# Performance work log

Measured on AMD Instinct MI355X. Metric: run time of the kernel, lower is better.

## Reference

```python
import jax, jax.numpy as jnp
import numpy as np

B, H, W = 8, 64, 64
DIM1, DIM2 = 384, 256
NH, DH = 8, 32
INNER = NH * DH
EPS = 1e-5


def _layernorm(x, w, b):
    mu = jnp.mean(x, axis=-1, keepdims=True)
    var = jnp.mean((x - mu) ** 2, axis=-1, keepdims=True)
    return (x - mu) * jax.lax.rsqrt(var + EPS) * w + b


def _axial_attn(q, k, v, scale):
    # q,k,v: [B,H,W,nh,dh]; row attention over H, col attention over W
    sh = jnp.einsum('biwnd,bjwnd->bwnij', q, k) * scale  # [B,W,nh,H,H]
    oh = jnp.einsum('bwnij,bjwnd->biwnd', jax.nn.softmax(sh, axis=-1), v)
    sw = jnp.einsum('bhind,bhjnd->bhnij', q, k) * scale  # [B,H,nh,W,W]
    ow = jnp.einsum('bhnij,bhjnd->bhind', jax.nn.softmax(sw, axis=-1), v)
    return oh + ow  # [B,H,W,nh,dh]


def setup_inputs() -> dict:
    key = jax.random.key(0)
    ks = jax.random.split(key, 16)
    s1 = 1.0 / np.sqrt(DIM1)
    s2 = 1.0 / np.sqrt(DIM2)
    si = 1.0 / np.sqrt(INNER)
    return {
        'x1': jax.random.normal(ks[0], (B, DIM1, H, W), jnp.float32),
        'x2': jax.random.normal(ks[1], (B, DIM2, H, W), jnp.float32),
        'ln1q_w': jnp.ones((DIM1,), jnp.float32),
        'ln1q_b': jnp.zeros((DIM1,), jnp.float32),
        'ln2kv_w': jnp.ones((DIM2,), jnp.float32),
        'ln2kv_b': jnp.zeros((DIM2,), jnp.float32),
        'Wq1': jax.random.normal(ks[2], (DIM1, INNER), jnp.float32) * s1,
        'Wkv2': jax.random.normal(ks[3], (DIM2, 2 * INNER), jnp.float32) * s2,
        'Wout1': jax.random.normal(ks[4], (INNER, DIM2), jnp.float32) * si,
        'bout1': jnp.zeros((DIM2,), jnp.float32),
        'ln2q_w': jnp.ones((DIM2,), jnp.float32),
        'ln2q_b': jnp.zeros((DIM2,), jnp.float32),
        'ln1kv_w': jnp.ones((DIM1,), jnp.float32),
        'ln1kv_b': jnp.zeros((DIM1,), jnp.float32),
        'Wq2': jax.random.normal(ks[5], (DIM2, INNER), jnp.float32) * s2,
        'Wkv1': jax.random.normal(ks[6], (DIM1, 2 * INNER), jnp.float32) * s1,
        'Wout2': jax.random.normal(ks[7], (INNER, DIM2), jnp.float32) * si,
        'bout2': jnp.zeros((DIM2,), jnp.float32),
        'Wsc': jax.random.normal(ks[8], (DIM2, DIM1), jnp.float32) * s1,  # 1x1 conv [out,in]
        'bn_gamma': jnp.ones((DIM2,), jnp.float32),
        'bn_beta': jnp.zeros((DIM2,), jnp.float32),
        'bn_mean': jnp.zeros((DIM2,), jnp.float32),
        'bn_var': jnp.ones((DIM2,), jnp.float32),
    }


def reference(x1, x2, ln1q_w, ln1q_b, ln2kv_w, ln2kv_b, Wq1, Wkv2, Wout1, bout1,
              ln2q_w, ln2q_b, ln1kv_w, ln1kv_b, Wq2, Wkv1, Wout2, bout2,
              Wsc, bn_gamma, bn_beta, bn_mean, bn_var):
    b, c1, h, w = x1.shape
    scale = DH ** -0.5
    x1f = jnp.transpose(x1, (0, 2, 3, 1))  # [B,H,W,C1]
    x2f = jnp.transpose(x2, (0, 2, 3, 1))  # [B,H,W,C2]

    def heads(t):
        return t.reshape(b, h, w, NH, DH)

    # branch 1: q from x1, kv from x2
    q1 = _layernorm(x1f, ln1q_w, ln1q_b) @ Wq1
    kv2 = _layernorm(x2f, ln2kv_w, ln2kv_b) @ Wkv2
    k2, v2 = jnp.split(kv2, 2, axis=-1)
    o1 = _axial_attn(heads(q1), heads(k2), heads(v2), scale)
    fused1 = o1.reshape(b, h, w, INNER) @ Wout1 + bout1
    # shortcut: 1x1 conv + BN (inference stats)
    sc = jnp.einsum('bhwc,oc->bhwo', x1f, Wsc)
    sc = (sc - bn_mean) * jax.lax.rsqrt(bn_var + EPS) * bn_gamma + bn_beta
    y1 = sc + fused1

    # branch 2: q from x2, kv from x1
    q2 = _layernorm(x2f, ln2q_w, ln2q_b) @ Wq2
    kv1 = _layernorm(x1f, ln1kv_w, ln1kv_b) @ Wkv1
    k1, v1 = jnp.split(kv1, 2, axis=-1)
    o2 = _axial_attn(heads(q2), heads(k1), heads(v1), scale)
    fused2 = o2.reshape(b, h, w, INNER) @ Wout2 + bout2
    y2 = x2f + fused2

    out = y1 + y2  # [B,H,W,C2]
    return jnp.transpose(out, (0, 3, 1, 2))
```

## Files before the change

### kernel.cpp

```cpp
#include <hip/hip_runtime.h>

typedef unsigned short u16;
typedef unsigned int u32;
typedef float v4f __attribute__((ext_vector_type(4)));
typedef __bf16 v8bf __attribute__((ext_vector_type(8)));
typedef short v4s __attribute__((ext_vector_type(4)));

__device__ __forceinline__ float bf2f(u16 v) {
  union { u32 u; float f; } x; x.u = ((u32)v) << 16; return x.f;
}
__device__ __forceinline__ u16 f2bf(float f) {
  union { float f; u32 u; } x; x.f = f;
  u32 u = x.u;
  return (u16)((u + 0x7FFFu + ((u >> 16) & 1u)) >> 16);
}
__device__ __forceinline__ u32 f2u(float f) {
  union { float f; u32 u; } x; x.f = f; return x.u;
}
__device__ __forceinline__ u32 pk2bf(float a, float b) {
  const u32 au = f2u(a) + 0x7FFFu + ((f2u(a) >> 16) & 1u);
  const u32 bu = f2u(b) + 0x7FFFu + ((f2u(b) >> 16) & 1u);
  return (bu & 0xFFFF0000u) | (au >> 16);
}
__device__ __forceinline__ u32 pk2bf_t(float a, float b) {
  return (f2u(b) & 0xFFFF0000u) | (f2u(a) >> 16);
}

__device__ __forceinline__ v4f mfma16(v4s a, v4s b, v4f c) {
#if __has_builtin(__builtin_amdgcn_mfma_f32_16x16x16bf16_1k)
  return __builtin_amdgcn_mfma_f32_16x16x16bf16_1k(a, b, c, 0, 0, 0);
#else
  v4f d = c;
  asm volatile("v_mfma_f32_16x16x16_bf16 %0, %1, %2, %0" : "+v"(d) : "v"(a), "v"(b));
  return d;
#endif
}

struct Ptrs { const void* p[23]; };

__global__ __launch_bounds__(256) void convert_all(Ptrs ps, u16* __restrict__ cx1,
                                                   u16* __restrict__ cx2,
                                                   u16* __restrict__ cw) {
  static const int sz[23]  = {12582912, 8388608, 384, 384, 256, 256, 98304, 131072,
                              65536, 256, 256, 256, 384, 384, 65536, 196608, 65536,
                              256, 98304, 256, 256, 256, 256};
  static const int off[23] = {0, 0, 0, 384, 768, 1024, 1280, 99584, 230656, 296192,
                              296448, 296704, 296960, 297344, 297728, 363264, 559872,
                              625408, 625664, 723968, 724224, 724480, 724736};
  const int ti = blockIdx.y;
  const int n8 = sz[ti] >> 3;
  const bool isf32 = (((const u32*)ps.p[2])[0] == 0x3F800000u);
  u16* dst = (ti == 0) ? cx1 : (ti == 1) ? cx2 : (cw + off[ti]);
  const void* src = ps.p[ti];
  const int stride = gridDim.x * blockDim.x;
  for (int i = blockIdx.x * blockDim.x + threadIdx.x; i < n8; i += stride) {
    if (isf32) {
      const float4 f0 = ((const float4*)src)[2*i];
      const float4 f1 = ((const float4*)src)[2*i + 1];
      u16 tmp[8];
      tmp[0] = f2bf(f0.x); tmp[1] = f2bf(f0.y); tmp[2] = f2bf(f0.z); tmp[3] = f2bf(f0.w);
      tmp[4] = f2bf(f1.x); tmp[5] = f2bf(f1.y); tmp[6] = f2bf(f1.z); tmp[7] = f2bf(f1.w);
      ((uint4*)dst)[i] = *(const uint4*)tmp;
    } else {
      ((uint4*)dst)[i] = ((const uint4*)src)[i];
    }
  }
}

__global__ void prep_bt(const u16* __restrict__ lnq_w, const u16* __restrict__ lnq_b,
                        const u16* __restrict__ lnkv_w, const u16* __restrict__ lnkv_b,
                        const u16* __restrict__ Wq, const u16* __restrict__ Wkv,
                        u16* __restrict__ BT, float* __restrict__ bias) {
  const int C = blockDim.x;
  const int j = blockIdx.x;
  const int c = threadIdx.x;
  const float qscale = 0.25503482620929637f;
  float w, bco, wv;
  if (j < 256) { w = bf2f(lnq_w[c]) * qscale; bco = bf2f(lnq_b[c]) * qscale; wv = bf2f(Wq[c*256 + j]); }
  else         { w = bf2f(lnkv_w[c]); bco = bf2f(lnkv_b[c]); wv = bf2f(Wkv[c*512 + (j-256)]); }
  BT[(size_t)j*C + c] = f2bf(w * wv);
  __shared__ float red[384];
  red[c] = bco * wv;
  __syncthreads();
  if (c == 0) { float s = 0.f; for (int i = 0; i < C; i++) s += red[i]; bias[j] = s; }
}

__global__ void prep_fin(const u16* __restrict__ Wout1, const u16* __restrict__ Wout2,
                         const u16* __restrict__ Wsc, const u16* __restrict__ bout1,
                         const u16* __restrict__ bout2, const u16* __restrict__ gam,
                         const u16* __restrict__ bet, const u16* __restrict__ mean,
                         const u16* __restrict__ var, u16* __restrict__ BT,
                         float* __restrict__ bias) {
  const int o = blockIdx.x, t = threadIdx.x;
  const float g = rsqrtf(bf2f(var[o]) + 1e-5f) * bf2f(gam[o]);
  for (int idx = t; idx < 1408; idx += 256) {
    float v;
    if (idx < 512)       v = bf2f(Wout1[(idx & 255)*256 + o]);
    else if (idx < 1024) v = bf2f(Wout2[((idx - 512) & 255)*256 + o]);
    else                 v = bf2f(Wsc[o*384 + (idx - 1024)]) * g;
    BT[(size_t)o*1408 + idx] = f2bf(v);
  }
  if (t == 0) bias[o] = bf2f(bet[o]) - bf2f(mean[o])*g + bf2f(bout1[o]) + bf2f(bout2[o]);
}

__global__ __launch_bounds__(256) void ln_c384(const u16* __restrict__ x,
                                               u16* __restrict__ xn, u16* __restrict__ xraw) {
  __shared__ u16 tile[384*66];
  __shared__ float rsum[4][64], rsq[4][64], smean[64], srstd[64];
  const int t = threadIdx.x, w = t & 63, g = t >> 6;
  const int bh = blockIdx.x, b = bh >> 6, h = bh & 63;
  const u16* src = x + (size_t)b*384*4096 + h*64 + w;
  float sum = 0.f, sq = 0.f;
  for (int j = 0; j < 96; j++) {
    const int c = g*96 + j;
    const u16 uv = src[(size_t)c*4096];
    tile[c*66 + w] = uv;
    const float v = bf2f(uv); sum += v; sq += v*v;
  }
  rsum[g][w] = sum; rsq[g][w] = sq;
  __syncthreads();
  if (t < 64) {
    const float s = rsum[0][t]+rsum[1][t]+rsum[2][t]+rsum[3][t];
    const float q = rsq[0][t]+rsq[1][t]+rsq[2][t]+rsq[3][t];
    const float mean = s * (1.0f/384.0f);
    float var = q * (1.0f/384.0f) - mean*mean;
    if (var < 0.f) var = 0.f;
    smean[t] = mean; srstd[t] = rsqrtf(var + 1e-5f);
  }
  __syncthreads();
  const size_t pos0 = (size_t)bh * 64;
  for (int i = 0; i < 96; i++) {
    const int flat = i*256 + t;
    const int ww = flat / 384, c = flat - ww*384;
    const u16 uv = tile[c*66 + ww];
    const float v = (bf2f(uv) - smean[ww]) * srstd[ww];
    const size_t p = pos0 + ww;
    xn[p*384 + c] = f2bf(v);
    xraw[p*384 + c] = uv;
  }
}

__global__ __launch_bounds__(256) void ln_c256(const u16* __restrict__ x,
                                               u16* __restrict__ xn) {
  __shared__ u16 tile[256*66];
  __shared__ float rsum[4][64], rsq[4][64], smean[64], srstd[64];
  const int t = threadIdx.x, w = t & 63, g = t >> 6;
  const int bh = blockIdx.x, b = bh >> 6, h = bh & 63;
  const u16* src = x + (size_t)b*256*4096 + h*64 + w;
  float sum = 0.f, sq = 0.f;
  for (int j = 0; j < 64; j++) {
    const int c = g*64 + j;
    const u16 uv = src[(size_t)c*4096];
    tile[c*66 + w] = uv;
    const float v = bf2f(uv); sum += v; sq += v*v;
  }
  rsum[g][w] = sum; rsq[g][w] = sq;
  __syncthreads();
  if (t < 64) {
    const float s = rsum[0][t]+rsum[1][t]+rsum[2][t]+rsum[3][t];
    const float q = rsq[0][t]+rsq[1][t]+rsq[2][t]+rsq[3][t];
    const float mean = s * (1.0f/256.0f);
    float var = q * (1.0f/256.0f) - mean*mean;
    if (var < 0.f) var = 0.f;
    smean[t] = mean; srstd[t] = rsqrtf(var + 1e-5f);
  }
  __syncthreads();
  const size_t pos0 = (size_t)bh * 64;
  for (int i = 0; i < 64; i++) {
    const int flat = i*256 + t;
    const int ww = flat >> 8, c = flat & 255;
    const float v = (bf2f(tile[c*66 + ww]) - smean[ww]) * srstd[ww];
    xn[(pos0 + ww)*256 + c] = f2bf(v);
  }
}

__global__ __launch_bounds__(512) void gemm_bt(const u16* __restrict__ A,
                                               const u16* __restrict__ BT,
                                               u16* __restrict__ C,
                                               const float* __restrict__ bias,
                                               int N, int K) {
  __shared__ u16 lsA[128*40];
  __shared__ u16 lsB[128*40];
  const int t = threadIdx.x;
  const int m0 = blockIdx.x * 128, n0 = blockIdx.y * 128;
  const int lane = t & 63, wv = t >> 6;
  const int wm = wv >> 1, wn = wv & 1;
  const int lo = lane & 15, hi = lane >> 4;
  const int r0 = t >> 2, c8 = (t & 3) << 3;
  const u16* Ab = A + (size_t)(m0 + r0) * K + c8;
  const u16* Bb = BT + (size_t)(n0 + r0) * K + c8;
  uint4 a = *(const uint4*)(Ab);
  uint4 bq = *(const uint4*)(Bb);
  v4f acc[2][4] = {};
  for (int kb = 0; kb < K; kb += 32) {
    __syncthreads();
    *(uint4*)&lsA[r0*40 + c8] = a;
    *(uint4*)&lsB[r0*40 + c8] = bq;
    __syncthreads();
    if (kb + 32 < K) {
      a = *(const uint4*)(Ab + kb + 32);
      bq = *(const uint4*)(Bb + kb + 32);
    }
    v8bf av[2], bv[4];
#pragma unroll
    for (int i = 0; i < 2; i++) av[i] = *(const v8bf*)&lsA[(wm*32 + i*16 + lo)*40 + hi*8];
#pragma unroll
    for (int i = 0; i < 4; i++) bv[i] = *(const v8bf*)&lsB[(wn*64 + i*16 + lo)*40 + hi*8];
#pragma unroll
    for (int mt = 0; mt < 2; mt++)
#pragma unroll
      for (int nt = 0; nt < 4; nt++)
        acc[mt][nt] = __builtin_amdgcn_mfma_f32_16x16x32_bf16(av[mt], bv[nt], acc[mt][nt], 0, 0, 0);
  }
#pragma unroll
  for (int mt = 0; mt < 2; mt++) {
    const int row = m0 + wm*32 + mt*16 + hi*4;
#pragma unroll
    for (int nt = 0; nt < 4; nt++) {
      const int col = n0 + wn*64 + nt*16 + lo;
      const float bs = bias[col];
#pragma unroll
      for (int r = 0; r < 4; r++)
        C[(size_t)(row + r) * N + col] = f2bf(acc[mt][nt][r] + bs);
    }
  }
}

__global__ __launch_bounds__(512) void gemm_final(const u16* __restrict__ Ao,
                                                  const u16* __restrict__ Ar,
                                                  const u16* __restrict__ BT,
                                                  const float* __restrict__ bias,
                                                  const u16* __restrict__ x2c,
                                                  const u32* __restrict__ probe,
                                                  void* __restrict__ outv) {
  __shared__ u16 smem[16640];
  u16* lsA = smem;
  u16* lsB = smem + 5120;
  const int t = threadIdx.x;
  const int m0 = blockIdx.x * 128, n0 = blockIdx.y * 128;
  const int lane = t & 63, wv = t >> 6;
  const int wm = wv >> 1, wn = wv & 1;
  const int lo = lane & 15, hi = lane >> 4;
  const int r0 = t >> 2, c8 = (t & 3) << 3;
  const u16* ArR = Ar + (size_t)(m0 + r0) * 384 + c8;
  const u16* Bb  = BT + (size_t)(n0 + r0) * 1408 + c8;

  uint4 a, bq;
  {
    a = *(const uint4*)(Ao + ((size_t)(0) * 32768 + m0 + r0) * 32 + c8);
    bq = *(const uint4*)(Bb);
  }
  v4f acc[2][4] = {};
  for (int kb = 0; kb < 1408; kb += 32) {
    __syncthreads();
    *(uint4*)&lsA[r0*40 + c8] = a;
    *(uint4*)&lsB[r0*40 + c8] = bq;
    __syncthreads();
    const int kn = kb + 32;
    if (kn < 1408) {
      if (kn < 1024) a = *(const uint4*)(Ao + ((size_t)(kn >> 5) * 32768 + m0 + r0) * 32 + c8);
      else           a = *(const uint4*)(ArR + (kn - 1024));
      bq = *(const uint4*)(Bb + kn);
    }
    v8bf av[2], bv[4];
#pragma unroll
    for (int i = 0; i < 2; i++) av[i] = *(const v8bf*)&lsA[(wm*32 + i*16 + lo)*40 + hi*8];
#pragma unroll
    for (int i = 0; i < 4; i++) bv[i] = *(const v8bf*)&lsB[(wn*64 + i*16 + lo)*40 + hi*8];
#pragma unroll
    for (int mt = 0; mt < 2; mt++)
#pragma unroll
      for (int nt = 0; nt < 4; nt++)
        acc[mt][nt] = __builtin_amdgcn_mfma_f32_16x16x32_bf16(av[mt], bv[nt], acc[mt][nt], 0, 0, 0);
  }
  __syncthreads();
#pragma unroll
  for (int mt = 0; mt < 2; mt++)
#pragma unroll
    for (int nt = 0; nt < 4; nt++) {
      const int nl = wn*64 + nt*16 + lo;
      const float bs = bias[n0 + nl];
#pragma unroll
      for (int r = 0; r < 4; r++)
        smem[(wm*32 + mt*16 + hi*4 + r)*130 + nl] = f2bf(acc[mt][nt][r] + bs);
    }
  __syncthreads();
  const bool isf32 = (probe[0] == 0x3F800000u);
  const int bh0 = blockIdx.x * 2;
  for (int i = 0; i < 32; i++) {
    const int flat = i*512 + t;
    const int nl = flat >> 7;
    const int rem = flat & 127;
    const int mb = rem >> 6, w = rem & 63;
    const int bh = bh0 + mb, b = bh >> 6, h = bh & 63;
    const size_t oidx = ((size_t)(b*256 + n0 + nl)*64 + h)*64 + w;
    const float val = bf2f(smem[(mb*64 + w)*130 + nl]) + bf2f(x2c[oidx]);
    if (isf32) ((float*)outv)[oidx] = val;
    else       ((u16*)outv)[oidx]   = f2bf(val);
  }
}

__global__ __launch_bounds__(512) void attn(const u16* __restrict__ qkv1,
                                            const u16* __restrict__ qkv2,
                                            u16* __restrict__ Ao) {
  __shared__ __attribute__((aligned(16))) u16 smem[8 * 2560];
  const int t = threadIdx.x;
  const int head = t >> 6, lane = t & 63;
  const int lo = lane & 15, quad = lane >> 4;
  u16* sw = smem + head * 2560;
  const int bx = blockIdx.x;
  const int z = blockIdx.y;
  const int br = z >> 1, dir = z & 1;
  const int b = bx >> 6, x = bx & 63;
  const u16* Qb  = (br == 0) ? qkv1 : qkv2;
  const u16* KVb = (br == 0) ? qkv2 : qkv1;
  const int qc = head*32, kc = 256 + head*32, vc = 512 + head*32;
  const int pbase = (dir == 0) ? (b*4096 + x) : ((b*64 + x)*64);
  const int pstr  = (dir == 0) ? 64 : 1;

  {
    const u16* vr = KVb + (size_t)(pbase + lane*pstr)*768 + vc;
    u16 vbuf[32];
#pragma unroll
    for (int i = 0; i < 4; i++) *(uint4*)&vbuf[i*8] = *(const uint4*)(vr + i*8);
    const int khi = lane >> 3, klo = lane & 7;
#pragma unroll
    for (int d = 0; d < 32; d++)
      sw[d*64 + ((khi ^ (d & 7)) << 3) + klo] = vbuf[d];
  }
  __syncthreads();

  v8bf qa[4], ka[4];
#pragma unroll
  for (int i = 0; i < 4; i++) {
    const size_t p = (size_t)(pbase + (i*16 + lo)*pstr) * 768;
    qa[i] = *(const v8bf*)(Qb + p + qc + quad*8);
    ka[i] = *(const v8bf*)(KVb + p + kc + quad*8);
  }

  v4f s[4][4];
  __builtin_amdgcn_s_setprio(1);
#pragma unroll
  for (int qt = 0; qt < 4; qt++)
#pragma unroll
    for (int kt = 0; kt < 4; kt++) {
      v4f z4 = {};
      s[qt][kt] = __builtin_amdgcn_mfma_f32_16x16x32_bf16(ka[kt], qa[qt], z4, 0, 0, 0);
    }
  __builtin_amdgcn_s_setprio(0);

  v4s va16[2][4];
#pragma unroll
  for (int mt = 0; mt < 2; mt++)
#pragma unroll
    for (int kt = 0; kt < 4; kt++) {
      const int d = mt*16 + lo;
      va16[mt][kt] = *(const v4s*)&sw[d*64 + (((2*kt + (quad >> 1)) ^ (d & 7)) << 3) + (quad & 1)*4];
    }

  v4f o[2][4] = {};
  float inv4[4];
#pragma unroll
  for (int qt = 0; qt < 4; qt++) {
    float tv[16];
    float mx = -1e30f;
#pragma unroll
    for (int kt = 0; kt < 4; kt++)
#pragma unroll
      for (int r = 0; r < 4; r++) {
        const float v = s[qt][kt][r];
        tv[kt*4 + r] = v;
        mx = fmaxf(mx, v);
      }
    mx = fmaxf(mx, __shfl_xor(mx, 16));
    mx = fmaxf(mx, __shfl_xor(mx, 32));
    float sm = 0.f;
#pragma unroll
    for (int i = 0; i < 16; i++) { tv[i] = exp2f(tv[i] - mx); sm += tv[i]; }
    sm += __shfl_xor(sm, 16);
    sm += __shfl_xor(sm, 32);
    inv4[qt] = 1.0f / sm;
    __builtin_amdgcn_s_setprio(1);
#pragma unroll
    for (int kt = 0; kt < 4; kt++) {
      union { u32 u[2]; v4s v; } pb;
      pb.u[0] = pk2bf_t(tv[kt*4 + 0], tv[kt*4 + 1]);
      pb.u[1] = pk2bf_t(tv[kt*4 + 2], tv[kt*4 + 3]);
#pragma unroll
      for (int mt = 0; mt < 2; mt++)
        o[mt][qt] = mfma16(va16[mt][kt], pb.v, o[mt][qt]);
    }
    __builtin_amdgcn_s_setprio(0);
  }

  __syncthreads();
#pragma unroll
  for (int mt = 0; mt < 2; mt++)
#pragma unroll
    for (int nt = 0; nt < 4; nt++)
#pragma unroll
      for (int rp = 0; rp < 2; rp++) {
        const u32 pkv = pk2bf(o[mt][nt][rp*2] * inv4[nt], o[mt][nt][rp*2 + 1] * inv4[nt]);
        *(u32*)&sw[(nt*16 + lo)*40 + mt*16 + quad*4 + rp*2] = pkv;
      }
  __syncthreads();
  {
    const size_t sbase = (size_t)(z*8 + head) * 32768 + pbase;
#pragma unroll
    for (int it = 0; it < 4; it++) {
      const int chunk = it*64 + lane;
      const int row = chunk >> 2, ic = chunk & 3;
      *(uint4*)&Ao[(sbase + (size_t)row*pstr)*32 + ic*8] = *(const uint4*)&sw[row*40 + ic*8];
    }
  }
}

extern "C" void kernel_launch(void* const* d_in, const int* in_sizes, int n_in,
                              void* d_out, int out_size, void* d_ws, size_t ws_size,
                              hipStream_t stream) {
  char* ws = (char*)d_ws;
  u16* Ao    = (u16*)(ws);
  u16* Araw  = (u16*)(ws + 67108864);
  u16* qkv1  = (u16*)(ws + 92274688);
  u16* qkv2  = (u16*)(ws + 142606336);
  u16* cx2   = (u16*)(ws + 192937984);
  u16* cw    = (u16*)(ws + 209715200);
  u16* BT1   = (u16*)(ws + 211165184);
  u16* BT2   = (u16*)(ws + 211755008);
  u16* BTf   = (u16*)(ws + 212148224);
  float* bias1 = (float*)(ws + 212869120);
  float* bias2 = (float*)(ws + 212872192);
  float* biasf = (float*)(ws + 212875264);
  u16* cx1 = qkv1;
  u16* x1n = Ao;
  u16* x2n = Ao + 12582912;

  u16* c_ln1q_w = cw + 0,     *c_ln1q_b = cw + 384;
  u16* c_ln2kv_w = cw + 768,  *c_ln2kv_b = cw + 1024;
  u16* c_Wq1 = cw + 1280,     *c_Wkv2 = cw + 99584;
  u16* c_Wout1 = cw + 230656, *c_bout1 = cw + 296192;
  u16* c_ln2q_w = cw + 296448,*c_ln2q_b = cw + 296704;
  u16* c_ln1kv_w = cw + 296960,*c_ln1kv_b = cw + 297344;
  u16* c_Wq2 = cw + 297728,   *c_Wkv1 = cw + 363264;
  u16* c_Wout2 = cw + 559872, *c_bout2 = cw + 625408;
  u16* c_Wsc = cw + 625664;
  u16* c_bn_g = cw + 723968,  *c_bn_b = cw + 724224;
  u16* c_bn_m = cw + 724480,  *c_bn_v = cw + 724736;

  Ptrs ps;
  for (int i = 0; i < 23; i++) ps.p[i] = d_in[i];

  convert_all<<<dim3(512, 23), 256, 0, stream>>>(ps, cx1, cx2, cw);
  prep_bt<<<768, 384, 0, stream>>>(c_ln1q_w, c_ln1q_b, c_ln1kv_w, c_ln1kv_b, c_Wq1, c_Wkv1, BT1, bias1);
  prep_bt<<<768, 256, 0, stream>>>(c_ln2q_w, c_ln2q_b, c_ln2kv_w, c_ln2kv_b, c_Wq2, c_Wkv2, BT2, bias2);
  prep_fin<<<256, 256, 0, stream>>>(c_Wout1, c_Wout2, c_Wsc, c_bout1, c_bout2,
                                    c_bn_g, c_bn_b, c_bn_m, c_bn_v, BTf, biasf);
  ln_c384<<<512, 256, 0, stream>>>(cx1, x1n, Araw);
  ln_c256<<<512, 256, 0, stream>>>(cx2, x2n);
  gemm_bt<<<dim3(256, 6), 512, 0, stream>>>(x1n, BT1, qkv1, bias1, 768, 384);
  gemm_bt<<<dim3(256, 6), 512, 0, stream>>>(x2n, BT2, qkv2, bias2, 768, 256);
  attn<<<dim3(512, 4), 512, 0, stream>>>(qkv1, qkv2, Ao);
  gemm_final<<<dim3(256, 2), 512, 0, stream>>>(Ao, Araw, BTf, biasf, cx2,
                                               (const u32*)d_in[2], d_out);
}
```

Baseline: 354.4 us.

## Double-buffer GEMM LDS tiles, split attention blocks by head, parallelize bias reduce

Both the QKV GEMM and the final GEMM now use two LDS stages and process two K-slices per iteration. This halves the barrier count and overlaps the global loads for the next slice with MFMA work on the current one. The attention kernel moves from 512-thread blocks covering 8 heads to 256-thread blocks covering 4 heads, with twice as many blocks, aiming for better occupancy and scheduling granularity. The prep_bt bias sum changes from a serial single-thread loop to a 64-lane strided sum plus a wavefront shuffle reduction.

```diff
diff --git a/kernel.cpp b/kernel.cpp
--- a/kernel.cpp
+++ b/kernel.cpp
@@ -82,7 +82,13 @@
   __shared__ float red[384];
   red[c] = bco * wv;
   __syncthreads();
-  if (c == 0) { float s = 0.f; for (int i = 0; i < C; i++) s += red[i]; bias[j] = s; }
+  if (c < 64) {
+    float s = 0.f;
+    for (int i = c; i < C; i += 64) s += red[i];
+#pragma unroll
+    for (int offd = 32; offd; offd >>= 1) s += __shfl_down(s, offd);
+    if (c == 0) bias[j] = s;
+  }
 }
 
 __global__ void prep_fin(const u16* __restrict__ Wout1, const u16* __restrict__ Wout2,
@@ -179,8 +185,7 @@
                                                u16* __restrict__ C,
                                                const float* __restrict__ bias,
                                                int N, int K) {
-  __shared__ u16 lsA[128*40];
-  __shared__ u16 lsB[128*40];
+  __shared__ u16 smem[20480];
   const int t = threadIdx.x;
   const int m0 = blockIdx.x * 128, n0 = blockIdx.y * 128;
   const int lane = t & 63, wv = t >> 6;
@@ -189,29 +194,47 @@
   const int r0 = t >> 2, c8 = (t & 3) << 3;
   const u16* Ab = A + (size_t)(m0 + r0) * K + c8;
   const u16* Bb = BT + (size_t)(n0 + r0) * K + c8;
-  uint4 a = *(const uint4*)(Ab);
-  uint4 bq = *(const uint4*)(Bb);
+  const int st = r0*40 + c8;
   v4f acc[2][4] = {};
-  for (int kb = 0; kb < K; kb += 32) {
+
+#define GBT_COMPUTE(BASE)                                                          \
+  {                                                                                \
+    v8bf av[2], bv[4];                                                             \
+    _Pragma("unroll")                                                              \
+    for (int i = 0; i < 2; i++) av[i] = *(const v8bf*)&smem[(BASE) + (wm*32 + i*16 + lo)*40 + hi*8]; \
+    _Pragma("unroll")                                                              \
+    for (int i = 0; i < 4; i++) bv[i] = *(const v8bf*)&smem[(BASE) + 5120 + (wn*64 + i*16 + lo)*40 + hi*8]; \
+    _Pragma("unroll")                                                              \
+    for (int mt = 0; mt < 2; mt++)                                                 \
+      _Pragma("unroll")                                                            \
+      for (int nt = 0; nt < 4; nt++)                                               \
+        acc[mt][nt] = __builtin_amdgcn_mfma_f32_16x16x32_bf16(av[mt], bv[nt], acc[mt][nt], 0, 0, 0); \
+  }
+
+  uint4 aA = *(const uint4*)(Ab);
+  uint4 bA = *(const uint4*)(Bb);
+  uint4 aB = *(const uint4*)(Ab + 32);
+  uint4 bB = *(const uint4*)(Bb + 32);
+  *(uint4*)&smem[st] = aA;
+  *(uint4*)&smem[5120 + st] = bA;
+  __syncthreads();
+
+  for (int kb = 0; kb < K; kb += 64) {
+    if (kb + 64 < K) { aA = *(const uint4*)(Ab + kb + 64); bA = *(const uint4*)(Bb + kb + 64); }
+    GBT_COMPUTE(0)
+    *(uint4*)&smem[10240 + st] = aB;
+    *(uint4*)&smem[15360 + st] = bB;
     __syncthreads();
-    *(uint4*)&lsA[r0*40 + c8] = a;
-    *(uint4*)&lsB[r0*40 + c8] = bq;
+    if (kb + 96 < K) { aB = *(const uint4*)(Ab + kb + 96); bB = *(const uint4*)(Bb + kb + 96); }
+    GBT_COMPUTE(10240)
+    if (kb + 64 < K) {
+      *(uint4*)&smem[st] = aA;
+      *(uint4*)&smem[5120 + st] = bA;
+    }
     __syncthreads();
-    if (kb + 32 < K) {
-      a = *(const uint4*)(Ab + kb + 32);
-      bq = *(const uint4*)(Bb + kb + 32);
-    }
-    v8bf av[2], bv[4];
-#pragma unroll
-    for (int i = 0; i < 2; i++) av[i] = *(const v8bf*)&lsA[(wm*32 + i*16 + lo)*40 + hi*8];
-#pragma unroll
-    for (int i = 0; i < 4; i++) bv[i] = *(const v8bf*)&lsB[(wn*64 + i*16 + lo)*40 + hi*8];
-#pragma unroll
-    for (int mt = 0; mt < 2; mt++)
-#pragma unroll
-      for (int nt = 0; nt < 4; nt++)
-        acc[mt][nt] = __builtin_amdgcn_mfma_f32_16x16x32_bf16(av[mt], bv[nt], acc[mt][nt], 0, 0, 0);
-  }
+  }
+#undef GBT_COMPUTE
+
 #pragma unroll
   for (int mt = 0; mt < 2; mt++) {
     const int row = m0 + wm*32 + mt*16 + hi*4;
@@ -233,9 +256,7 @@
                                                   const u16* __restrict__ x2c,
                                                   const u32* __restrict__ probe,
                                                   void* __restrict__ outv) {
-  __shared__ u16 smem[16640];
-  u16* lsA = smem;
-  u16* lsB = smem + 5120;
+  __shared__ u16 smem[20480];
   const int t = threadIdx.x;
   const int m0 = blockIdx.x * 128, n0 = blockIdx.y * 128;
   const int lane = t & 63, wv = t >> 6;
@@ -244,36 +265,50 @@
   const int r0 = t >> 2, c8 = (t & 3) << 3;
   const u16* ArR = Ar + (size_t)(m0 + r0) * 384 + c8;
   const u16* Bb  = BT + (size_t)(n0 + r0) * 1408 + c8;
-
-  uint4 a, bq;
-  {
-    a = *(const uint4*)(Ao + ((size_t)(0) * 32768 + m0 + r0) * 32 + c8);
-    bq = *(const uint4*)(Bb);
-  }
+  const int st = r0*40 + c8;
   v4f acc[2][4] = {};
-  for (int kb = 0; kb < 1408; kb += 32) {
+
+#define GF_LOADA(KB) ((KB) < 1024 ? *(const uint4*)(Ao + ((size_t)((KB) >> 5) * 32768 + m0 + r0) * 32 + c8) \
+                                  : *(const uint4*)(ArR + ((KB) - 1024)))
+#define GF_COMPUTE(BASE)                                                           \
+  {                                                                                \
+    v8bf av[2], bv[4];                                                             \
+    _Pragma("unroll")                                                              \
+    for (int i = 0; i < 2; i++) av[i] = *(const v8bf*)&smem[(BASE) + (wm*32 + i*16 + lo)*40 + hi*8]; \
+    _Pragma("unroll")                                                              \
+    for (int i = 0; i < 4; i++) bv[i] = *(const v8bf*)&smem[(BASE) + 5120 + (wn*64 + i*16 + lo)*40 + hi*8]; \
+    _Pragma("unroll")                                                              \
+    for (int mt = 0; mt < 2; mt++)                                                 \
+      _Pragma("unroll")                                                            \
+      for (int nt = 0; nt < 4; nt++)                                               \
+        acc[mt][nt] = __builtin_amdgcn_mfma_f32_16x16x32_bf16(av[mt], bv[nt], acc[mt][nt], 0, 0, 0); \
+  }
+
+  uint4 aA = GF_LOADA(0);
+  uint4 bA = *(const uint4*)(Bb);
+  uint4 aB = GF_LOADA(32);
+  uint4 bB = *(const uint4*)(Bb + 32);
+  *(uint4*)&smem[st] = aA;
+  *(uint4*)&smem[5120 + st] = bA;
+  __syncthreads();
+
+  for (int kb = 0; kb < 1408; kb += 64) {
+    if (kb + 64 < 1408) { aA = GF_LOADA(kb + 64); bA = *(const uint4*)(Bb + kb + 64); }
+    GF_COMPUTE(0)
+    *(uint4*)&smem[10240 + st] = aB;
+    *(uint4*)&smem[15360 + st] = bB;
     __syncthreads();
-    *(uint4*)&lsA[r0*40 + c8] = a;
-    *(uint4*)&lsB[r0*40 + c8] = bq;
+    if (kb + 96 < 1408) { aB = GF_LOADA(kb + 96); bB = *(const uint4*)(Bb + kb + 96); }
+    GF_COMPUTE(10240)
+    if (kb + 64 < 1408) {
+      *(uint4*)&smem[st] = aA;
+      *(uint4*)&smem[5120 + st] = bA;
+    }
     __syncthreads();
-    const int kn = kb + 32;
-    if (kn < 1408) {
-      if (kn < 1024) a = *(const uint4*)(Ao + ((size_t)(kn >> 5) * 32768 + m0 + r0) * 32 + c8);
-      else           a = *(const uint4*)(ArR + (kn - 1024));
-      bq = *(const uint4*)(Bb + kn);
-    }
-    v8bf av[2], bv[4];
-#pragma unroll
-    for (int i = 0; i < 2; i++) av[i] = *(const v8bf*)&lsA[(wm*32 + i*16 + lo)*40 + hi*8];
-#pragma unroll
-    for (int i = 0; i < 4; i++) bv[i] = *(const v8bf*)&lsB[(wn*64 + i*16 + lo)*40 + hi*8];
-#pragma unroll
-    for (int mt = 0; mt < 2; mt++)
-#pragma unroll
-      for (int nt = 0; nt < 4; nt++)
-        acc[mt][nt] = __builtin_amdgcn_mfma_f32_16x16x32_bf16(av[mt], bv[nt], acc[mt][nt], 0, 0, 0);
-  }
-  __syncthreads();
+  }
+#undef GF_COMPUTE
+#undef GF_LOADA
+
 #pragma unroll
   for (int mt = 0; mt < 2; mt++)
 #pragma unroll
@@ -300,16 +335,16 @@
   }
 }
 
-__global__ __launch_bounds__(512) void attn(const u16* __restrict__ qkv1,
+__global__ __launch_bounds__(256) void attn(const u16* __restrict__ qkv1,
                                             const u16* __restrict__ qkv2,
                                             u16* __restrict__ Ao) {
-  __shared__ __attribute__((aligned(16))) u16 smem[8 * 2560];
+  __shared__ __attribute__((aligned(16))) u16 smem[4 * 2560];
   const int t = threadIdx.x;
-  const int head = t >> 6, lane = t & 63;
+  const int head = ((blockIdx.y & 1) << 2) + (t >> 6), lane = t & 63;
   const int lo = lane & 15, quad = lane >> 4;
-  u16* sw = smem + head * 2560;
+  u16* sw = smem + (t >> 6) * 2560;
   const int bx = blockIdx.x;
-  const int z = blockIdx.y;
+  const int z = blockIdx.y >> 1;
   const int br = z >> 1, dir = z & 1;
   const int b = bx >> 6, x = bx & 63;
   const u16* Qb  = (br == 0) ? qkv1 : qkv2;
@@ -459,7 +494,7 @@
   ln_c256<<<512, 256, 0, stream>>>(cx2, x2n);
   gemm_bt<<<dim3(256, 6), 512, 0, stream>>>(x1n, BT1, qkv1, bias1, 768, 384);
   gemm_bt<<<dim3(256, 6), 512, 0, stream>>>(x2n, BT2, qkv2, bias2, 768, 256);
-  attn<<<dim3(512, 4), 512, 0, stream>>>(qkv1, qkv2, Ao);
+  attn<<<dim3(512, 8), 256, 0, stream>>>(qkv1, qkv2, Ao);
   gemm_final<<<dim3(256, 2), 512, 0, stream>>>(Ao, Araw, BTf, biasf, cx2,
                                                (const u32*)d_in[2], d_out);
 }
```

Measured after the change: 351.0 us. About the same (-1.0%).

## Use direct global-to-LDS loads in GEMMs, split attention blocks, parallelize bias reduction

Applied to the files above, without the earlier changes.

Both GEMM kernels now stage A and B tiles with global_load_lds straight into XOR-swizzled LDS instead of going through registers with padded rows. This drops the register round trip and the next-tile register prefetch, so the load is no longer overlapped with the current tile's MFMAs. The attention kernel moves to 256-thread blocks of 4 heads on a doubled grid, and the V transpose store into LDS now happens after the Q/K global loads are issued. The prep_bt bias sum moves from a serial loop on one thread to a 64-lane shuffle reduction.

```diff
diff --git a/kernel.cpp b/kernel.cpp
--- a/kernel.cpp
+++ b/kernel.cpp
@@ -34,6 +34,12 @@
   asm volatile("v_mfma_f32_16x16x16_bf16 %0, %1, %2, %0" : "+v"(d) : "v"(a), "v"(b));
   return d;
 #endif
+}
+
+__device__ __forceinline__ void gl_lds16(const void* g, void* l) {
+  __builtin_amdgcn_global_load_lds(
+      (const __attribute__((address_space(1))) void*)g,
+      (__attribute__((address_space(3))) void*)l, 16, 0, 0);
 }
 
 struct Ptrs { const void* p[23]; };
@@ -82,7 +88,13 @@
   __shared__ float red[384];
   red[c] = bco * wv;
   __syncthreads();
-  if (c == 0) { float s = 0.f; for (int i = 0; i < C; i++) s += red[i]; bias[j] = s; }
+  if (c < 64) {
+    float s = 0.f;
+    for (int i = c; i < C; i += 64) s += red[i];
+#pragma unroll
+    for (int offd = 32; offd; offd >>= 1) s += __shfl_down(s, offd);
+    if (c == 0) bias[j] = s;
+  }
 }
 
 __global__ void prep_fin(const u16* __restrict__ Wout1, const u16* __restrict__ Wout2,
@@ -179,33 +191,35 @@
                                                u16* __restrict__ C,
                                                const float* __restrict__ bias,
                                                int N, int K) {
-  __shared__ u16 lsA[128*40];
-  __shared__ u16 lsB[128*40];
+  __shared__ __attribute__((aligned(16))) u16 smem[8192];
   const int t = threadIdx.x;
   const int m0 = blockIdx.x * 128, n0 = blockIdx.y * 128;
   const int lane = t & 63, wv = t >> 6;
   const int wm = wv >> 1, wn = wv & 1;
   const int lo = lane & 15, hi = lane >> 4;
-  const int r0 = t >> 2, c8 = (t & 3) << 3;
-  const u16* Ab = A + (size_t)(m0 + r0) * K + c8;
-  const u16* Bb = BT + (size_t)(n0 + r0) * K + c8;
-  uint4 a = *(const uint4*)(Ab);
-  uint4 bq = *(const uint4*)(Bb);
+  const int srow = wv*16 + (lane >> 2);
+  const int sslot = (lane & 3) ^ (srow & 3);
+  const u16* Ag = A + (size_t)(m0 + srow) * K + sslot*8;
+  const u16* Bg = BT + (size_t)(n0 + srow) * K + sslot*8;
+  u16* lA = &smem[wv * 512];
+  u16* lB = &smem[4096 + wv * 512];
   v4f acc[2][4] = {};
   for (int kb = 0; kb < K; kb += 32) {
     __syncthreads();
-    *(uint4*)&lsA[r0*40 + c8] = a;
-    *(uint4*)&lsB[r0*40 + c8] = bq;
+    gl_lds16(Ag + kb, lA);
+    gl_lds16(Bg + kb, lB);
     __syncthreads();
-    if (kb + 32 < K) {
-      a = *(const uint4*)(Ab + kb + 32);
-      bq = *(const uint4*)(Bb + kb + 32);
-    }
     v8bf av[2], bv[4];
 #pragma unroll
-    for (int i = 0; i < 2; i++) av[i] = *(const v8bf*)&lsA[(wm*32 + i*16 + lo)*40 + hi*8];
-#pragma unroll
-    for (int i = 0; i < 4; i++) bv[i] = *(const v8bf*)&lsB[(wn*64 + i*16 + lo)*40 + hi*8];
+    for (int i = 0; i < 2; i++) {
+      const int r = wm*32 + i*16 + lo;
+      av[i] = *(const v8bf*)&smem[r*32 + ((hi ^ (r & 3)) << 3)];
+    }
+#pragma unroll
+    for (int i = 0; i < 4; i++) {
+      const int r = wn*64 + i*16 + lo;
+      bv[i] = *(const v8bf*)&smem[4096 + r*32 + ((hi ^ (r & 3)) << 3)];
+    }
 #pragma unroll
     for (int mt = 0; mt < 2; mt++)
 #pragma unroll
@@ -233,40 +247,38 @@
                                                   const u16* __restrict__ x2c,
                                                   const u32* __restrict__ probe,
                                                   void* __restrict__ outv) {
-  __shared__ u16 smem[16640];
-  u16* lsA = smem;
-  u16* lsB = smem + 5120;
+  __shared__ __attribute__((aligned(16))) u16 smem[16640];
   const int t = threadIdx.x;
   const int m0 = blockIdx.x * 128, n0 = blockIdx.y * 128;
   const int lane = t & 63, wv = t >> 6;
   const int wm = wv >> 1, wn = wv & 1;
   const int lo = lane & 15, hi = lane >> 4;
-  const int r0 = t >> 2, c8 = (t & 3) << 3;
-  const u16* ArR = Ar + (size_t)(m0 + r0) * 384 + c8;
-  const u16* Bb  = BT + (size_t)(n0 + r0) * 1408 + c8;
-
-  uint4 a, bq;
-  {
-    a = *(const uint4*)(Ao + ((size_t)(0) * 32768 + m0 + r0) * 32 + c8);
-    bq = *(const uint4*)(Bb);
-  }
+  const int srow = wv*16 + (lane >> 2);
+  const int sslot = (lane & 3) ^ (srow & 3);
+  const u16* ArR = Ar + (size_t)(m0 + srow) * 384 + sslot*8;
+  const u16* AoR = Ao + ((size_t)(m0 + srow)) * 32 + sslot*8;
+  const u16* Bg  = BT + (size_t)(n0 + srow) * 1408 + sslot*8;
+  u16* lA = &smem[wv * 512];
+  u16* lB = &smem[4096 + wv * 512];
   v4f acc[2][4] = {};
   for (int kb = 0; kb < 1408; kb += 32) {
     __syncthreads();
-    *(uint4*)&lsA[r0*40 + c8] = a;
-    *(uint4*)&lsB[r0*40 + c8] = bq;
+    const u16* ga = (kb < 1024) ? (AoR + (size_t)(kb >> 5) * 32768 * 32)
+                                : (ArR + (kb - 1024));
+    gl_lds16(ga, lA);
+    gl_lds16(Bg + kb, lB);
     __syncthreads();
-    const int kn = kb + 32;
-    if (kn < 1408) {
-      if (kn < 1024) a = *(const uint4*)(Ao + ((size_t)(kn >> 5) * 32768 + m0 + r0) * 32 + c8);
-      else           a = *(const uint4*)(ArR + (kn - 1024));
-      bq = *(const uint4*)(Bb + kn);
-    }
     v8bf av[2], bv[4];
 #pragma unroll
-    for (int i = 0; i < 2; i++) av[i] = *(const v8bf*)&lsA[(wm*32 + i*16 + lo)*40 + hi*8];
-#pragma unroll
-    for (int i = 0; i < 4; i++) bv[i] = *(const v8bf*)&lsB[(wn*64 + i*16 + lo)*40 + hi*8];
+    for (int i = 0; i < 2; i++) {
+      const int r = wm*32 + i*16 + lo;
+      av[i] = *(const v8bf*)&smem[r*32 + ((hi ^ (r & 3)) << 3)];
+    }
+#pragma unroll
+    for (int i = 0; i < 4; i++) {
+      const int r = wn*64 + i*16 + lo;
+      bv[i] = *(const v8bf*)&smem[4096 + r*32 + ((hi ^ (r & 3)) << 3)];
+    }
 #pragma unroll
     for (int mt = 0; mt < 2; mt++)
 #pragma unroll
@@ -300,16 +312,16 @@
   }
 }
 
-__global__ __launch_bounds__(512) void attn(const u16* __restrict__ qkv1,
+__global__ __launch_bounds__(256) void attn(const u16* __restrict__ qkv1,
                                             const u16* __restrict__ qkv2,
                                             u16* __restrict__ Ao) {
-  __shared__ __attribute__((aligned(16))) u16 smem[8 * 2560];
+  __shared__ __attribute__((aligned(16))) u16 smem[4 * 2560];
   const int t = threadIdx.x;
-  const int head = t >> 6, lane = t & 63;
+  const int head = ((blockIdx.y & 1) << 2) + (t >> 6), lane = t & 63;
   const int lo = lane & 15, quad = lane >> 4;
-  u16* sw = smem + head * 2560;
+  u16* sw = smem + (t >> 6) * 2560;
   const int bx = blockIdx.x;
-  const int z = blockIdx.y;
+  const int z = blockIdx.y >> 1;
   const int br = z >> 1, dir = z & 1;
   const int b = bx >> 6, x = bx & 63;
   const u16* Qb  = (br == 0) ? qkv1 : qkv2;
@@ -318,18 +330,12 @@
   const int pbase = (dir == 0) ? (b*4096 + x) : ((b*64 + x)*64);
   const int pstr  = (dir == 0) ? 64 : 1;
 
+  u16 vbuf[32];
   {
     const u16* vr = KVb + (size_t)(pbase + lane*pstr)*768 + vc;
-    u16 vbuf[32];
 #pragma unroll
     for (int i = 0; i < 4; i++) *(uint4*)&vbuf[i*8] = *(const uint4*)(vr + i*8);
-    const int khi = lane >> 3, klo = lane & 7;
-#pragma unroll
-    for (int d = 0; d < 32; d++)
-      sw[d*64 + ((khi ^ (d & 7)) << 3) + klo] = vbuf[d];
-  }
-  __syncthreads();
-
+  }
   v8bf qa[4], ka[4];
 #pragma unroll
   for (int i = 0; i < 4; i++) {
@@ -337,6 +343,14 @@
     qa[i] = *(const v8bf*)(Qb + p + qc + quad*8);
     ka[i] = *(const v8bf*)(KVb + p + kc + quad*8);
   }
+
+  {
+    const int khi = lane >> 3, klo = lane & 7;
+#pragma unroll
+    for (int d = 0; d < 32; d++)
+      sw[d*64 + ((khi ^ (d & 7)) << 3) + klo] = vbuf[d];
+  }
+  __syncthreads();
 
   v4f s[4][4];
   __builtin_amdgcn_s_setprio(1);
@@ -459,7 +473,7 @@
   ln_c256<<<512, 256, 0, stream>>>(cx2, x2n);
   gemm_bt<<<dim3(256, 6), 512, 0, stream>>>(x1n, BT1, qkv1, bias1, 768, 384);
   gemm_bt<<<dim3(256, 6), 512, 0, stream>>>(x2n, BT2, qkv2, bias2, 768, 256);
-  attn<<<dim3(512, 4), 512, 0, stream>>>(qkv1, qkv2, Ao);
+  attn<<<dim3(512, 8), 256, 0, stream>>>(qkv1, qkv2, Ao);
   gemm_final<<<dim3(256, 2), 512, 0, stream>>>(Ao, Araw, BTf, biasf, cx2,
                                                (const u32*)d_in[2], d_out);
 }
```

Result: faster. 345.0 us (-2.7%).
